# Optimization experiments

Hardware: AMD Instinct MI355X
Metric: run time of the kernel (lower is better)

Reference implementation:

```python
import jax, jax.numpy as jnp
import numpy as np

BOS = 1
MAX_LEN = 20


def _lstm_cell(x, h, c, Wih, Whh, bih, bhh):
    # torch.nn.LSTMCell gate order: i, f, g, o
    g = x @ Wih.T + h @ Whh.T + bih + bhh
    i, f, gg, o = jnp.split(g, 4, axis=-1)
    c = jax.nn.sigmoid(f) * c + jax.nn.sigmoid(i) * jnp.tanh(gg)
    h = jax.nn.sigmoid(o) * jnp.tanh(c)
    return h, c


def setup_inputs() -> dict:
    key = jax.random.key(0)
    ks = jax.random.split(key, 12)
    B, K, D = 512, 36, 2048
    A, H, Em, V = 512, 512, 300, 10000
    s = 0.02
    rn = lambda k, shape, sc=s: sc * jax.random.normal(k, shape, dtype=jnp.float32)
    return {
        'feats': jax.random.normal(ks[0], (B, K, D), dtype=jnp.float32),
        'Wp': rn(ks[1], (A, D)), 'bp': jnp.zeros((A,), jnp.float32),
        'E': rn(ks[2], (V, Em), 0.1).at[0].set(0.0),  # padding_idx = 0
        'Wih1': rn(ks[3], (4 * H, Em + A)), 'Whh1': rn(ks[4], (4 * H, H)),
        'bih1': jnp.zeros((4 * H,), jnp.float32), 'bhh1': jnp.zeros((4 * H,), jnp.float32),
        'Wih2': rn(ks[5], (4 * H, H + A)), 'Whh2': rn(ks[6], (4 * H, H)),
        'bih2': jnp.zeros((4 * H,), jnp.float32), 'bhh2': jnp.zeros((4 * H,), jnp.float32),
        'Wa1': rn(ks[7], (A, H + A)), 'ba1': jnp.zeros((A,), jnp.float32),
        'wa2': rn(ks[8], (1, A)), 'ba2': jnp.zeros((1,), jnp.float32),
        'Wo': rn(ks[9], (V, H)), 'bo': jnp.zeros((V,), jnp.float32),
    }


def reference(feats, Wp, bp, E, Wih1, Whh1, bih1, bhh1, Wih2, Whh2, bih2, bhh2,
              Wa1, ba1, wa2, ba2, Wo, bo):
    B, K, D = feats.shape
    H = Whh1.shape[1]
    f_att = feats @ Wp.T + bp                      # [B, K, A]
    f_mean = f_att.mean(axis=1)                    # [B, A]
    # attn Linear over concat([h1, f_att]): split columns, precompute f_att term
    Wa1_h, Wa1_f = Wa1[:, :H], Wa1[:, H:]
    att_f = f_att @ Wa1_f.T + ba1                  # [B, K, A]
    x0 = jnp.broadcast_to(E[BOS], (B, E.shape[1]))
    z = jnp.zeros((B, H), jnp.float32)
    carry0 = (x0, z, z, z, z)

    def step(carry, _):
        x, h1, c1, h2, c2 = carry
        h1, c1 = _lstm_cell(jnp.concatenate([x, f_mean], axis=-1), h1, c1,
                            Wih1, Whh1, bih1, bhh1)
        pre = jnp.tanh(att_f + (h1 @ Wa1_h.T)[:, None, :])   # [B, K, A]
        e = pre @ wa2[0] + ba2[0]                            # [B, K]
        alpha = jax.nn.softmax(e, axis=-1)
        ctx = jnp.einsum('bk,bka->ba', alpha, f_att)         # [B, A]
        h2, c2 = _lstm_cell(jnp.concatenate([h1, ctx], axis=-1), h2, c2,
                            Wih2, Whh2, bih2, bhh2)
        logit = h2 @ Wo.T + bo                               # [B, V]  (dropout is identity in eval)
        nxt = jnp.argmax(logit, axis=-1)
        return (E[nxt], h1, c1, h2, c2), nxt

    _, ids = jax.lax.scan(step, carry0, None, length=MAX_LEN - 1)
    return ids.T  # [B, MAX_LEN-1], matches torch.stack(out_ids, 1)
```

## Files before the change

### kernel.cpp

```cpp
#include <hip/hip_runtime.h>
#include <math.h>
#include <stdint.h>

constexpr int Bsz = 512, Kf = 36, Dd = 2048, Aa = 512, Hh = 512, Em = 300;
constexpr int Vv = 10000, TSTEPS = 19, BOS = 1;
constexpr int K1 = 832;
constexpr int K2 = 1536;
constexpr int VvP = 10112;
constexpr float SPLIT_S  = 2048.0f;
constexpr float SPLIT_IS = 1.0f / 2048.0f;

#define CDIV(a,b) (((a)+(b)-1)/(b))

typedef _Float16 f16x8 __attribute__((ext_vector_type(8)));
typedef float    f32x4 __attribute__((ext_vector_type(4)));

typedef const unsigned int GU __attribute__((address_space(1)));
typedef unsigned int       LU __attribute__((address_space(3)));

__device__ __forceinline__ void gload16(const void* g, void* l) {
    __builtin_amdgcn_global_load_lds((GU*)g, (LU*)l, 16, 0, 0);
}

template<int N> __device__ __forceinline__ void wait_vm() {
    if constexpr (N == 0)       asm volatile("s_waitcnt vmcnt(0)" ::: "memory");
    else if constexpr (N == 4)  asm volatile("s_waitcnt vmcnt(4)" ::: "memory");
    else if constexpr (N == 6)  asm volatile("s_waitcnt vmcnt(6)" ::: "memory");
    else if constexpr (N == 8)  asm volatile("s_waitcnt vmcnt(8)" ::: "memory");
    else if constexpr (N == 12) asm volatile("s_waitcnt vmcnt(12)" ::: "memory");
    else if constexpr (N == 16) asm volatile("s_waitcnt vmcnt(16)" ::: "memory");
    else static_assert(N == 0, "unsupported vmcnt literal");
}
#define WAIT_LGKM asm volatile("s_waitcnt lgkmcnt(0)" ::: "memory")
#define SB0 __builtin_amdgcn_sched_barrier(0)
#define BAR __builtin_amdgcn_s_barrier()

__device__ __forceinline__ float sigm(float v) { return 1.0f / (1.0f + expf(-v)); }

__device__ __forceinline__ void wsplit(_Float16* __restrict__ hi, _Float16* __restrict__ lo,
                                       size_t idx, float v) {
    _Float16 h = (_Float16)v;
    hi[idx] = h;
    lo[idx] = (_Float16)((v - (float)h) * SPLIT_S);
}

template<int BM, int BN, int BK, bool AF32>
__global__ __launch_bounds__(256)
void gemm_sp(const float* __restrict__ Af,
             const _Float16* __restrict__ Ahi, const _Float16* __restrict__ Alo, int lda,
             const _Float16* __restrict__ Bhi, const _Float16* __restrict__ Blo, int ldb,
             float* __restrict__ C, int ldc, int N, int K,
             const float* __restrict__ bias1, const float* __restrict__ bias2,
             const float* __restrict__ addC)
{
    constexpr int WM = BM / 2, WN = BN / 2;
    constexpr int MF = WM / 16, NF = WN / 16;
    constexpr int PA  = BK / 8;
    constexpr int PSA = BM * 8 + 8;
    constexpr int PSB = BN * 8 + 8;
    constexpr int SZA = PA * PSA, SZB = PA * PSB;
    constexpr int OAH = 0, OAL = SZA, OBH = 2 * SZA, OBL = 2 * SZA + SZB;
    constexpr int BUF = 2 * SZA + 2 * SZB;
    constexpr int NCHA = BM * BK / 2048;
    constexpr int NCHB = BN * BK / 2048;
    constexpr int LW = 2 * NCHA + 2 * NCHB;
    __shared__ _Float16 sm[2 * BUF];

    const int t    = threadIdx.x;
    const int lane = t & 63;
    const int w    = t >> 6;
    const int wr   = w >> 1, wc = w & 1;
    const int m0   = blockIdx.y * BM, n0 = blockIdx.x * BN;
    const int l15  = lane & 15, l4 = lane >> 4;

    f32x4 acch[MF][NF];
    f32x4 accm[MF][NF];
    #pragma unroll
    for (int m = 0; m < MF; ++m)
        #pragma unroll
        for (int n = 0; n < NF; ++n) {
            acch[m][n] = (f32x4){0.f, 0.f, 0.f, 0.f};
            accm[m][n] = (f32x4){0.f, 0.f, 0.f, 0.f};
        }

    const int nkt = K / BK;

    auto stageB = [&](int bufo, int kt) {
        #pragma unroll
        for (int i = 0; i < NCHB; ++i) {
            const int q  = i * 256 + t;
            const int p  = q / BN, r = q % BN;
            const int qw = i * 256 + (t & ~63);
            const int pu = qw / BN, ru = qw % BN;
            const size_t goff = (size_t)(n0 + r) * ldb + kt * BK + p * 8;
            gload16(Bhi + goff, &sm[bufo + OBH + pu * PSB + ru * 8]);
            gload16(Blo + goff, &sm[bufo + OBL + pu * PSB + ru * 8]);
        }
    };
    auto stageA16 = [&](int bufo, int kt) {
        #pragma unroll
        for (int i = 0; i < NCHA; ++i) {
            const int q  = i * 256 + t;
            const int p  = q / BM, r = q % BM;
            const int qw = i * 256 + (t & ~63);
            const int pu = qw / BM, ru = qw % BM;
            const size_t goff = (size_t)(m0 + r) * lda + kt * BK + p * 8;
            gload16(Ahi + goff, &sm[bufo + OAH + pu * PSA + ru * 8]);
            gload16(Alo + goff, &sm[bufo + OAL + pu * PSA + ru * 8]);
        }
    };
    auto issueA = [&](float4 (&rd)[NCHA][2], int kt) {
        #pragma unroll
        for (int i = 0; i < NCHA; ++i) {
            const int q = i * 256 + t;
            const int p = q / BM, r = q % BM;
            const float* src = Af + (size_t)(m0 + r) * lda + kt * BK + p * 8;
            rd[i][0] = *(const float4*)src;
            rd[i][1] = *(const float4*)(src + 4);
        }
    };
    auto writeA = [&](int bufo, float4 (&rd)[NCHA][2]) {
        #pragma unroll
        for (int i = 0; i < NCHA; ++i) {
            const int q = i * 256 + t;
            const int p = q / BM, r = q % BM;
            const float f[8] = {rd[i][0].x, rd[i][0].y, rd[i][0].z, rd[i][0].w,
                                rd[i][1].x, rd[i][1].y, rd[i][1].z, rd[i][1].w};
            f16x8 hi, lo;
            #pragma unroll
            for (int j = 0; j < 8; ++j) {
                _Float16 h = (_Float16)f[j];
                hi[j] = h;
                lo[j] = (_Float16)((f[j] - (float)h) * SPLIT_S);
            }
            *(f16x8*)&sm[bufo + OAH + p * PSA + r * 8] = hi;
            *(f16x8*)&sm[bufo + OAL + p * PSA + r * 8] = lo;
        }
    };
    auto compute = [&](int bufo) {
        #pragma unroll
        for (int s = 0; s < BK / 32; ++s) {
            f16x8 ah[MF], al[MF], bh[NF], bl[NF];
            const int pl = s * 4 + l4;
            #pragma unroll
            for (int m = 0; m < MF; ++m) {
                const int row = wr * WM + m * 16 + l15;
                ah[m] = *(const f16x8*)&sm[bufo + OAH + pl * PSA + row * 8];
                al[m] = *(const f16x8*)&sm[bufo + OAL + pl * PSA + row * 8];
            }
            #pragma unroll
            for (int n = 0; n < NF; ++n) {
                const int row = wc * WN + n * 16 + l15;
                bh[n] = *(const f16x8*)&sm[bufo + OBH + pl * PSB + row * 8];
                bl[n] = *(const f16x8*)&sm[bufo + OBL + pl * PSB + row * 8];
            }
            #pragma unroll
            for (int m = 0; m < MF; ++m)
                #pragma unroll
                for (int n = 0; n < NF; ++n) {
                    acch[m][n] = __builtin_amdgcn_mfma_f32_16x16x32_f16(ah[m], bh[n], acch[m][n], 0, 0, 0);
                    accm[m][n] = __builtin_amdgcn_mfma_f32_16x16x32_f16(ah[m], bl[n], accm[m][n], 0, 0, 0);
                    accm[m][n] = __builtin_amdgcn_mfma_f32_16x16x32_f16(al[m], bh[n], accm[m][n], 0, 0, 0);
                }
        }
    };

    if constexpr (AF32) {
        float4 rA[NCHA][2], rB[NCHA][2];
        issueA(rA, 0); stageB(0, 0);
        for (int kt = 0; kt < nkt; kt += 2) {
            issueA(rB, kt + 1); stageB(BUF, kt + 1);
            wait_vm<LW>(); SB0;
            writeA(0, rA);
            WAIT_LGKM; SB0;
            BAR; SB0;
            compute(0);
            SB0; WAIT_LGKM; BAR; SB0;
            if (kt + 2 < nkt) { issueA(rA, kt + 2); stageB(0, kt + 2); wait_vm<LW>(); }
            else              { wait_vm<0>(); }
            SB0;
            writeA(BUF, rB);
            WAIT_LGKM; SB0;
            BAR; SB0;
            compute(BUF);
            SB0; WAIT_LGKM; BAR; SB0;
        }
    } else {
        stageA16(0, 0); stageB(0, 0);
        for (int kt = 0; kt < nkt; ++kt) {
            const int bufc = (kt & 1) ? BUF : 0;
            const int bufn = BUF - bufc;
            if (kt + 1 < nkt) { stageA16(bufn, kt + 1); stageB(bufn, kt + 1); wait_vm<LW>(); }
            else              { wait_vm<0>(); }
            SB0;
            BAR; SB0;
            compute(bufc);
            SB0; WAIT_LGKM; BAR; SB0;
        }
    }

    #pragma unroll
    for (int m = 0; m < MF; ++m) {
        const int rowb = m0 + wr * WM + m * 16 + l4 * 4;
        #pragma unroll
        for (int n = 0; n < NF; ++n) {
            const int col = n0 + wc * WN + n * 16 + l15;
            if (col < N) {
                float bb = 0.f;
                if (bias1) bb += bias1[col];
                if (bias2) bb += bias2[col];
                #pragma unroll
                for (int r = 0; r < 4; ++r) {
                    const size_t idx = (size_t)(rowb + r) * ldc + col;
                    float v = acch[m][n][r] + accm[m][n][r] * SPLIT_IS + bb;
                    if (addC) v += addC[idx];
                    C[idx] = v;
                }
            }
        }
    }
}

__global__ __launch_bounds__(256)
void split_convert(const float* __restrict__ src, int srcld, int validR,
                   _Float16* __restrict__ dhi, _Float16* __restrict__ dlo,
                   int dstld, int coloff, int R, int C)
{
    const int total = R * C;
    for (int i = blockIdx.x * 256 + threadIdx.x; i < total; i += gridDim.x * 256) {
        const int r = i / C, c = i % C;
        const float v = (r < validR) ? src[(size_t)r * srcld + c] : 0.f;
        wsplit(dhi, dlo, (size_t)r * dstld + coloff + c, v);
    }
}

__global__ __launch_bounds__(256)
void init_kernel(_Float16* __restrict__ a1h, _Float16* __restrict__ a1l,
                 _Float16* __restrict__ a2h, _Float16* __restrict__ a2l,
                 float* __restrict__ c1, float* __restrict__ c2,
                 const float* __restrict__ E)
{
    const int idx = blockIdx.x * 256 + threadIdx.x;
    if (idx < Bsz * K1) {
        const int col = idx % K1;
        const float v = (col < Em) ? E[(size_t)BOS * Em + col] : 0.f;
        wsplit(a1h, a1l, idx, v);
    }
    if (idx < Bsz * K2) wsplit(a2h, a2l, idx, 0.f);
    if (idx < Bsz * Hh) { c1[idx] = 0.f; c2[idx] = 0.f; }
}

__global__ __launch_bounds__(256)
void fmean_kernel(const float* __restrict__ f_att, float* __restrict__ f_mean,
                  _Float16* __restrict__ fmh, _Float16* __restrict__ fml)
{
    const int b = blockIdx.x;
    for (int a = threadIdx.x; a < Aa; a += 256) {
        float s = 0.f;
        for (int k = 0; k < Kf; ++k) s += f_att[((size_t)b * Kf + k) * Aa + a];
        const float v = s * (1.0f / 36.0f);
        f_mean[(size_t)b * Aa + a] = v;
        wsplit(fmh, fml, (size_t)b * Aa + a, v);
    }
}

__global__ __launch_bounds__(256)
void lstm_cell_kernel(const float* __restrict__ g, float* __restrict__ c,
                      _Float16* __restrict__ hhi, _Float16* __restrict__ hlo,
                      int hld, int hoff,
                      _Float16* __restrict__ h2hi, _Float16* __restrict__ h2lo,
                      int h2ld, int h2off)
{
    const int idx = blockIdx.x * 256 + threadIdx.x;
    const int b = idx >> 9, h = idx & 511;
    const float* gb = g + (size_t)b * 2048;
    const float gi = gb[h], gf = gb[512 + h], gc = gb[1024 + h], go = gb[1536 + h];
    const float cv = sigm(gf) * c[idx] + sigm(gi) * tanhf(gc);
    c[idx] = cv;
    const float hv = sigm(go) * tanhf(cv);
    wsplit(hhi, hlo, (size_t)b * hld + hoff + h, hv);
    if (h2hi) wsplit(h2hi, h2lo, (size_t)b * h2ld + h2off + h, hv);
}

__global__ __launch_bounds__(256)
void attn_fused(const float* __restrict__ att_f, const float* __restrict__ q,
                const float* __restrict__ wa2, const float* __restrict__ ba2,
                const float* __restrict__ f_att,
                _Float16* __restrict__ a2h, _Float16* __restrict__ a2l)
{
    const int b = blockIdx.x, tid = threadIdx.x;
    const int w = tid >> 6, lane = tid & 63;
    __shared__ float se[Kf];
    __shared__ float wk[Kf];
    const float* pq = q + (size_t)b * Aa;
    for (int k = w; k < Kf; k += 4) {
        const float* pf = att_f + ((size_t)b * Kf + k) * Aa;
        float s = 0.f;
        #pragma unroll
        for (int j = 0; j < Aa; j += 64) {
            const int a = j + lane;
            s += tanhf(pf[a] + pq[a]) * wa2[a];
        }
        #pragma unroll
        for (int off = 32; off; off >>= 1) s += __shfl_down(s, off);
        if (lane == 0) se[k] = s + ba2[0];
    }
    __syncthreads();
    if (tid < Kf) {
        float mx = -INFINITY;
        for (int k = 0; k < Kf; ++k) mx = fmaxf(mx, se[k]);
        float ssum = 0.f;
        for (int k = 0; k < Kf; ++k) ssum += expf(se[k] - mx);
        wk[tid] = expf(se[tid] - mx) / ssum;
    }
    __syncthreads();
    for (int a = tid; a < Aa; a += 256) {
        float acc = 0.f;
        for (int k = 0; k < Kf; ++k)
            acc = fmaf(wk[k], f_att[((size_t)b * Kf + k) * Aa + a], acc);
        wsplit(a2h, a2l, (size_t)b * K2 + Hh + a, acc);
    }
}

__global__ __launch_bounds__(256)
void argmax_embed_kernel(const float* __restrict__ logits, const float* __restrict__ E,
                         _Float16* __restrict__ a1h, _Float16* __restrict__ a1l,
                         int* __restrict__ out, int t)
{
    const int b = blockIdx.x;
    const int tid = threadIdx.x;
    float best = -INFINITY;
    int bi = Vv;
    for (int j = tid; j < Vv; j += 256) {
        const float v = logits[(size_t)b * Vv + j];
        if (v > best) { best = v; bi = j; }
    }
    __shared__ float sv[256];
    __shared__ int   si[256];
    sv[tid] = best; si[tid] = bi;
    __syncthreads();
    for (int s = 128; s > 0; s >>= 1) {
        if (tid < s) {
            const float v2 = sv[tid + s];
            const int   i2 = si[tid + s];
            if (v2 > sv[tid] || (v2 == sv[tid] && i2 < si[tid])) { sv[tid] = v2; si[tid] = i2; }
        }
        __syncthreads();
    }
    const int idx = si[0];
    if (tid == 0) out[(size_t)b * TSTEPS + t] = idx;
    for (int d = tid; d < Em; d += 256)
        wsplit(a1h, a1l, (size_t)b * K1 + d, E[(size_t)idx * Em + d]);
}

static inline void conv(hipStream_t s, const float* src, int srcld, int validR,
                        _Float16* dhi, _Float16* dlo, int dstld, int coloff, int R, int C)
{
    int blocks = CDIV(R * C, 256); if (blocks > 2048) blocks = 2048;
    split_convert<<<dim3(blocks), dim3(256), 0, s>>>(src, srcld, validR, dhi, dlo, dstld, coloff, R, C);
}

extern "C" void kernel_launch(void* const* d_in, const int* in_sizes, int n_in,
                              void* d_out, int out_size, void* d_ws, size_t ws_size,
                              hipStream_t stream)
{
    const float* feats = (const float*)d_in[0];
    const float* Wp    = (const float*)d_in[1];
    const float* bp    = (const float*)d_in[2];
    const float* E     = (const float*)d_in[3];
    const float* Wih1  = (const float*)d_in[4];
    const float* Whh1  = (const float*)d_in[5];
    const float* bih1  = (const float*)d_in[6];
    const float* bhh1  = (const float*)d_in[7];
    const float* Wih2  = (const float*)d_in[8];
    const float* Whh2  = (const float*)d_in[9];
    const float* bih2  = (const float*)d_in[10];
    const float* bhh2  = (const float*)d_in[11];
    const float* Wa1   = (const float*)d_in[12];
    const float* ba1   = (const float*)d_in[13];
    const float* wa2   = (const float*)d_in[14];
    const float* ba2   = (const float*)d_in[15];
    const float* Wo    = (const float*)d_in[16];
    const float* bo    = (const float*)d_in[17];
    int* out = (int*)d_out;
    (void)in_sizes; (void)n_in; (void)out_size; (void)ws_size;

    uint8_t* w = (uint8_t*)d_ws;
    size_t off = 0;
    auto alloc = [&](size_t bytes) { void* p = w + off; off = (off + bytes + 255) & ~(size_t)255; return p; };

    float*     f_att  = (float*)alloc(18432ull * 512 * 4);
    float*     att_f  = (float*)alloc(18432ull * 512 * 4);
    float*     f_mean = (float*)alloc(512ull * 512 * 4);
    _Float16*  fmh    = (_Float16*)alloc(512ull * 512 * 2);
    _Float16*  fml    = (_Float16*)alloc(512ull * 512 * 2);
    _Float16*  wph    = (_Float16*)alloc(512ull * 2048 * 2);
    _Float16*  wpl    = (_Float16*)alloc(512ull * 2048 * 2);
    _Float16*  w1ph   = (_Float16*)alloc(2048ull * K1 * 2);
    _Float16*  w1pl   = (_Float16*)alloc(2048ull * K1 * 2);
    _Float16*  w1ch   = (_Float16*)alloc(2048ull * 512 * 2);
    _Float16*  w1cl   = (_Float16*)alloc(2048ull * 512 * 2);
    _Float16*  w2ph   = (_Float16*)alloc(2048ull * K2 * 2);
    _Float16*  w2pl   = (_Float16*)alloc(2048ull * K2 * 2);
    _Float16*  wahh   = (_Float16*)alloc(512ull * 512 * 2);
    _Float16*  wahl   = (_Float16*)alloc(512ull * 512 * 2);
    _Float16*  wafh   = (_Float16*)alloc(512ull * 512 * 2);
    _Float16*  wafl   = (_Float16*)alloc(512ull * 512 * 2);
    _Float16*  woh    = (_Float16*)alloc((size_t)VvP * 512 * 2);
    _Float16*  wol    = (_Float16*)alloc((size_t)VvP * 512 * 2);
    float*     g1c    = (float*)alloc(512ull * 2048 * 4);
    _Float16*  a1h    = (_Float16*)alloc(512ull * K1 * 2);
    _Float16*  a1l    = (_Float16*)alloc(512ull * K1 * 2);
    _Float16*  a2h    = (_Float16*)alloc(512ull * K2 * 2);
    _Float16*  a2l    = (_Float16*)alloc(512ull * K2 * 2);
    float*     c1     = (float*)alloc(512ull * 512 * 4);
    float*     c2     = (float*)alloc(512ull * 512 * 4);
    float*     gbuf   = (float*)alloc(512ull * 2048 * 4);
    float*     qbuf   = (float*)alloc(512ull * 512 * 4);
    float*     logits = (float*)alloc(512ull * Vv * 4);

    conv(stream, Wp,          Dd,      512,   wph,  wpl,  2048, 0,    512,  2048);
    conv(stream, Wih1,        Em + Aa, 2048,  w1ph, w1pl, K1,   0,    2048, Em);
    conv(stream, Whh1,        Hh,      2048,  w1ph, w1pl, K1,   Em,   2048, 512);
    conv(stream, Wih1,        Em + Aa, 0,     w1ph, w1pl, K1,   812,  2048, 20);
    conv(stream, Wih1 + Em,   Em + Aa, 2048,  w1ch, w1cl, 512,  0,    2048, 512);
    conv(stream, Wih2,        Hh + Aa, 2048,  w2ph, w2pl, K2,   0,    2048, 1024);
    conv(stream, Whh2,        Hh,      2048,  w2ph, w2pl, K2,   1024, 2048, 512);
    conv(stream, Wa1,         Hh + Aa, 512,   wahh, wahl, 512,  0,    512,  512);
    conv(stream, Wa1 + Hh,    Hh + Aa, 512,   wafh, wafl, 512,  0,    512,  512);
    conv(stream, Wo,          Hh,      Vv,    woh,  wol,  512,  0,    VvP,  512);

    init_kernel<<<dim3(CDIV(Bsz * K2, 256)), dim3(256), 0, stream>>>(a1h, a1l, a2h, a2l, c1, c2, E);

    gemm_sp<128, 128, 32, true><<<dim3(4, 144), 256, 0, stream>>>(
        feats, nullptr, nullptr, Dd, wph, wpl, 2048, f_att, 512, 512, 2048, bp, nullptr, nullptr);
    fmean_kernel<<<dim3(Bsz), dim3(256), 0, stream>>>(f_att, f_mean, fmh, fml);
    gemm_sp<64, 64, 64, false><<<dim3(32, 8), 256, 0, stream>>>(
        nullptr, fmh, fml, 512, w1ch, w1cl, 512, g1c, 2048, 2048, 512, bih1, bhh1, nullptr);
    gemm_sp<128, 128, 32, true><<<dim3(4, 144), 256, 0, stream>>>(
        f_att, nullptr, nullptr, 512, wafh, wafl, 512, att_f, 512, 512, 512, ba1, nullptr, nullptr);

    for (int t = 0; t < TSTEPS; ++t) {
        gemm_sp<64, 64, 64, false><<<dim3(32, 8), 256, 0, stream>>>(
            nullptr, a1h, a1l, K1, w1ph, w1pl, K1, gbuf, 2048, 2048, K1, nullptr, nullptr, g1c);
        lstm_cell_kernel<<<dim3(Bsz * Hh / 256), dim3(256), 0, stream>>>(
            gbuf, c1, a2h, a2l, K2, 0, a1h, a1l, K1, Em);
        gemm_sp<64, 64, 64, false><<<dim3(8, 8), 256, 0, stream>>>(
            nullptr, a2h, a2l, K2, wahh, wahl, 512, qbuf, 512, 512, 512, nullptr, nullptr, nullptr);
        attn_fused<<<dim3(Bsz), dim3(256), 0, stream>>>(att_f, qbuf, wa2, ba2, f_att, a2h, a2l);
        gemm_sp<64, 64, 64, false><<<dim3(32, 8), 256, 0, stream>>>(
            nullptr, a2h, a2l, K2, w2ph, w2pl, K2, gbuf, 2048, 2048, K2, bih2, bhh2, nullptr);
        lstm_cell_kernel<<<dim3(Bsz * Hh / 256), dim3(256), 0, stream>>>(
            gbuf, c2, a2h, a2l, K2, 1024, nullptr, nullptr, 0, 0);
        gemm_sp<64, 64, 64, false><<<dim3(158, 8), 256, 0, stream>>>(
            nullptr, a2h + 1024, a2l + 1024, K2, woh, wol, 512, logits, Vv, Vv, 512, bo, nullptr, nullptr);
        argmax_embed_kernel<<<dim3(Bsz), dim3(256), 0, stream>>>(logits, E, a1h, a1l, out, t);
    }
}
```

Baseline: 3.604 ms.

## Retile split-fp16 GEMMs, remap workgroups for XCD locality, fuse query projection into attention

The GEMM kernel now takes a 1D grid and remaps block IDs so consecutive tiles land on the same XCD, with NFAST choosing the tile order. It also gains an occupancy hint in launch_bounds. Tile shapes change for every GEMM (128x64 for the feature projections, BK 32 for the recurrent GEMMs, 64x128 for the vocab projection). The per-step h1 @ Wa1_h GEMM launch is removed: attn_fused rebuilds h1 from the split halves and does the projection in fp32 against a transposed weight, which saves a launch and the qbuf round trip. The cost is redundant per-block matvec work over a 1MB weight, 512 times per step.

After: 3.778 ms. 1.05x slower.

```diff
diff --git a/kernel.cpp b/kernel.cpp
--- a/kernel.cpp
+++ b/kernel.cpp
@@ -27,8 +27,6 @@
     else if constexpr (N == 4)  asm volatile("s_waitcnt vmcnt(4)" ::: "memory");
     else if constexpr (N == 6)  asm volatile("s_waitcnt vmcnt(6)" ::: "memory");
     else if constexpr (N == 8)  asm volatile("s_waitcnt vmcnt(8)" ::: "memory");
-    else if constexpr (N == 12) asm volatile("s_waitcnt vmcnt(12)" ::: "memory");
-    else if constexpr (N == 16) asm volatile("s_waitcnt vmcnt(16)" ::: "memory");
     else static_assert(N == 0, "unsupported vmcnt literal");
 }
 #define WAIT_LGKM asm volatile("s_waitcnt lgkmcnt(0)" ::: "memory")
@@ -44,14 +42,14 @@
     lo[idx] = (_Float16)((v - (float)h) * SPLIT_S);
 }
 
-template<int BM, int BN, int BK, bool AF32>
-__global__ __launch_bounds__(256)
+template<int BM, int BN, int BK, bool AF32, bool NFAST, int OCC>
+__global__ __launch_bounds__(256, OCC)
 void gemm_sp(const float* __restrict__ Af,
              const _Float16* __restrict__ Ahi, const _Float16* __restrict__ Alo, int lda,
              const _Float16* __restrict__ Bhi, const _Float16* __restrict__ Blo, int ldb,
              float* __restrict__ C, int ldc, int N, int K,
              const float* __restrict__ bias1, const float* __restrict__ bias2,
-             const float* __restrict__ addC)
+             const float* __restrict__ addC, int gxn)
 {
     constexpr int WM = BM / 2, WN = BN / 2;
     constexpr int MF = WM / 16, NF = WN / 16;
@@ -66,11 +64,19 @@
     constexpr int LW = 2 * NCHA + 2 * NCHB;
     __shared__ _Float16 sm[2 * BUF];
 
+    const int nwg = gridDim.x;
+    const int cpx = nwg >> 3;
+    const int orig = blockIdx.x;
+    const int lid = (orig & 7) * cpx + (orig >> 3);
+    int mt, nt;
+    if (NFAST) { nt = lid % gxn; mt = lid / gxn; }
+    else       { const int gym = nwg / gxn; mt = lid % gym; nt = lid / gym; }
+    const int m0 = mt * BM, n0 = nt * BN;
+
     const int t    = threadIdx.x;
     const int lane = t & 63;
     const int w    = t >> 6;
     const int wr   = w >> 1, wc = w & 1;
-    const int m0   = blockIdx.y * BM, n0 = blockIdx.x * BN;
     const int l15  = lane & 15, l4 = lane >> 4;
 
     f32x4 acch[MF][NF];
@@ -235,6 +241,16 @@
 }
 
 __global__ __launch_bounds__(256)
+void transpose_wah(const float* __restrict__ Wa1, float* __restrict__ WahT)
+{
+    const int i = blockIdx.x * 256 + threadIdx.x;
+    if (i < Aa * Hh) {
+        const int a = i / Hh, h = i % Hh;
+        WahT[(size_t)h * Aa + a] = Wa1[(size_t)a * (Hh + Aa) + h];
+    }
+}
+
+__global__ __launch_bounds__(256)
 void init_kernel(_Float16* __restrict__ a1h, _Float16* __restrict__ a1l,
                  _Float16* __restrict__ a2h, _Float16* __restrict__ a2l,
                  float* __restrict__ c1, float* __restrict__ c2,
@@ -283,23 +299,36 @@
 }
 
 __global__ __launch_bounds__(256)
-void attn_fused(const float* __restrict__ att_f, const float* __restrict__ q,
+void attn_fused(const float* __restrict__ att_f,
+                const _Float16* __restrict__ a2hin, const _Float16* __restrict__ a2lin,
+                const float* __restrict__ WahT,
                 const float* __restrict__ wa2, const float* __restrict__ ba2,
                 const float* __restrict__ f_att,
                 _Float16* __restrict__ a2h, _Float16* __restrict__ a2l)
 {
     const int b = blockIdx.x, tid = threadIdx.x;
     const int w = tid >> 6, lane = tid & 63;
+    __shared__ float sh1[Hh];
+    __shared__ float sq[Aa];
     __shared__ float se[Kf];
     __shared__ float wk[Kf];
-    const float* pq = q + (size_t)b * Aa;
+    for (int h = tid; h < Hh; h += 256)
+        sh1[h] = (float)a2hin[(size_t)b * K2 + h] + (float)a2lin[(size_t)b * K2 + h] * SPLIT_IS;
+    __syncthreads();
+    for (int a = tid; a < Aa; a += 256) {
+        float acc = 0.f;
+        for (int h = 0; h < Hh; ++h)
+            acc = fmaf(sh1[h], WahT[(size_t)h * Aa + a], acc);
+        sq[a] = acc;
+    }
+    __syncthreads();
     for (int k = w; k < Kf; k += 4) {
         const float* pf = att_f + ((size_t)b * Kf + k) * Aa;
         float s = 0.f;
         #pragma unroll
         for (int j = 0; j < Aa; j += 64) {
             const int a = j + lane;
-            s += tanhf(pf[a] + pq[a]) * wa2[a];
+            s += tanhf(pf[a] + sq[a]) * wa2[a];
         }
         #pragma unroll
         for (int off = 32; off; off >>= 1) s += __shfl_down(s, off);
@@ -402,8 +431,7 @@
     _Float16*  w1cl   = (_Float16*)alloc(2048ull * 512 * 2);
     _Float16*  w2ph   = (_Float16*)alloc(2048ull * K2 * 2);
     _Float16*  w2pl   = (_Float16*)alloc(2048ull * K2 * 2);
-    _Float16*  wahh   = (_Float16*)alloc(512ull * 512 * 2);
-    _Float16*  wahl   = (_Float16*)alloc(512ull * 512 * 2);
+    float*     WahT   = (float*)alloc(512ull * 512 * 4);
     _Float16*  wafh   = (_Float16*)alloc(512ull * 512 * 2);
     _Float16*  wafl   = (_Float16*)alloc(512ull * 512 * 2);
     _Float16*  woh    = (_Float16*)alloc((size_t)VvP * 512 * 2);
@@ -416,7 +444,6 @@
     float*     c1     = (float*)alloc(512ull * 512 * 4);
     float*     c2     = (float*)alloc(512ull * 512 * 4);
     float*     gbuf   = (float*)alloc(512ull * 2048 * 4);
-    float*     qbuf   = (float*)alloc(512ull * 512 * 4);
     float*     logits = (float*)alloc(512ull * Vv * 4);
 
     conv(stream, Wp,          Dd,      512,   wph,  wpl,  2048, 0,    512,  2048);
@@ -426,34 +453,33 @@
     conv(stream, Wih1 + Em,   Em + Aa, 2048,  w1ch, w1cl, 512,  0,    2048, 512);
     conv(stream, Wih2,        Hh + Aa, 2048,  w2ph, w2pl, K2,   0,    2048, 1024);
     conv(stream, Whh2,        Hh,      2048,  w2ph, w2pl, K2,   1024, 2048, 512);
-    conv(stream, Wa1,         Hh + Aa, 512,   wahh, wahl, 512,  0,    512,  512);
+    transpose_wah<<<dim3(1024), dim3(256), 0, stream>>>(Wa1, WahT);
     conv(stream, Wa1 + Hh,    Hh + Aa, 512,   wafh, wafl, 512,  0,    512,  512);
     conv(stream, Wo,          Hh,      Vv,    woh,  wol,  512,  0,    VvP,  512);
 
     init_kernel<<<dim3(CDIV(Bsz * K2, 256)), dim3(256), 0, stream>>>(a1h, a1l, a2h, a2l, c1, c2, E);
 
-    gemm_sp<128, 128, 32, true><<<dim3(4, 144), 256, 0, stream>>>(
-        feats, nullptr, nullptr, Dd, wph, wpl, 2048, f_att, 512, 512, 2048, bp, nullptr, nullptr);
+    gemm_sp<128, 64, 32, true, true, 2><<<dim3(1152), 256, 0, stream>>>(
+        feats, nullptr, nullptr, Dd, wph, wpl, 2048, f_att, 512, 512, 2048, bp, nullptr, nullptr, 8);
     fmean_kernel<<<dim3(Bsz), dim3(256), 0, stream>>>(f_att, f_mean, fmh, fml);
-    gemm_sp<64, 64, 64, false><<<dim3(32, 8), 256, 0, stream>>>(
-        nullptr, fmh, fml, 512, w1ch, w1cl, 512, g1c, 2048, 2048, 512, bih1, bhh1, nullptr);
-    gemm_sp<128, 128, 32, true><<<dim3(4, 144), 256, 0, stream>>>(
-        f_att, nullptr, nullptr, 512, wafh, wafl, 512, att_f, 512, 512, 512, ba1, nullptr, nullptr);
+    gemm_sp<64, 64, 32, false, false, 4><<<dim3(256), 256, 0, stream>>>(
+        nullptr, fmh, fml, 512, w1ch, w1cl, 512, g1c, 2048, 2048, 512, bih1, bhh1, nullptr, 32);
+    gemm_sp<128, 64, 32, true, true, 2><<<dim3(1152), 256, 0, stream>>>(
+        f_att, nullptr, nullptr, 512, wafh, wafl, 512, att_f, 512, 512, 512, ba1, nullptr, nullptr, 8);
 
     for (int t = 0; t < TSTEPS; ++t) {
-        gemm_sp<64, 64, 64, false><<<dim3(32, 8), 256, 0, stream>>>(
-            nullptr, a1h, a1l, K1, w1ph, w1pl, K1, gbuf, 2048, 2048, K1, nullptr, nullptr, g1c);
+        gemm_sp<64, 64, 32, false, false, 4><<<dim3(256), 256, 0, stream>>>(
+            nullptr, a1h, a1l, K1, w1ph, w1pl, K1, gbuf, 2048, 2048, K1, nullptr, nullptr, g1c, 32);
         lstm_cell_kernel<<<dim3(Bsz * Hh / 256), dim3(256), 0, stream>>>(
             gbuf, c1, a2h, a2l, K2, 0, a1h, a1l, K1, Em);
-        gemm_sp<64, 64, 64, false><<<dim3(8, 8), 256, 0, stream>>>(
-            nullptr, a2h, a2l, K2, wahh, wahl, 512, qbuf, 512, 512, 512, nullptr, nullptr, nullptr);
-        attn_fused<<<dim3(Bsz), dim3(256), 0, stream>>>(att_f, qbuf, wa2, ba2, f_att, a2h, a2l);
-        gemm_sp<64, 64, 64, false><<<dim3(32, 8), 256, 0, stream>>>(
-            nullptr, a2h, a2l, K2, w2ph, w2pl, K2, gbuf, 2048, 2048, K2, bih2, bhh2, nullptr);
+        attn_fused<<<dim3(Bsz), dim3(256), 0, stream>>>(
+            att_f, a2h, a2l, WahT, wa2, ba2, f_att, a2h, a2l);
+        gemm_sp<64, 64, 32, false, false, 4><<<dim3(256), 256, 0, stream>>>(
+            nullptr, a2h, a2l, K2, w2ph, w2pl, K2, gbuf, 2048, 2048, K2, bih2, bhh2, nullptr, 32);
         lstm_cell_kernel<<<dim3(Bsz * Hh / 256), dim3(256), 0, stream>>>(
             gbuf, c2, a2h, a2l, K2, 1024, nullptr, nullptr, 0, 0);
-        gemm_sp<64, 64, 64, false><<<dim3(158, 8), 256, 0, stream>>>(
-            nullptr, a2h + 1024, a2l + 1024, K2, woh, wol, 512, logits, Vv, Vv, 512, bo, nullptr, nullptr);
+        gemm_sp<64, 128, 32, false, false, 3><<<dim3(632), 256, 0, stream>>>(
+            nullptr, a2h + 1024, a2l + 1024, K2, woh, wol, 512, logits, Vv, Vv, 512, bo, nullptr, nullptr, 79);
         argmax_embed_kernel<<<dim3(Bsz), dim3(256), 0, stream>>>(logits, E, a1h, a1l, out, t);
     }
 }
```
